# Kernel tuning notes

Hardware: AMD Instinct MI355X
Metric: run time of the kernel (lower is better)

Reference implementation:

```python
import math
import jax, jax.numpy as jnp
import numpy as np

NUM_EXPERTS = 8
TOP_K = 2
CAPACITY_FACTOR = 1.0
B, S, H, I = 4, 2048, 1024, 4096


def setup_inputs() -> dict:
    key = jax.random.key(0)
    k_x, k_rw, k_wi, k_wo = jax.random.split(key, 4)
    x = jax.random.normal(k_x, (B, S, H), dtype=jnp.float32)
    # router: nn.Linear(H, E), xavier_uniform weight, zero-ish bias
    lim = math.sqrt(6.0 / (H + NUM_EXPERTS))
    router_w = jax.random.uniform(k_rw, (NUM_EXPERTS, H), minval=-lim, maxval=lim, dtype=jnp.float32)
    router_b = jnp.zeros((NUM_EXPERTS,), dtype=jnp.float32)
    # expert weights (scaled randn for numerical sanity)
    experts_inter = jax.random.normal(k_wi, (NUM_EXPERTS - 1, H, I), dtype=jnp.float32) / math.sqrt(H)
    experts_out = jax.random.normal(k_wo, (NUM_EXPERTS - 1, I, H), dtype=jnp.float32) / math.sqrt(I)
    return {"x": x, "router_w": router_w, "router_b": router_b,
            "experts_inter": experts_inter, "experts_out": experts_out}


def reference(x, router_w, router_b, experts_inter, experts_out):
    batch, seq, hidden = x.shape
    n_exp = router_w.shape[0]
    n_tok = batch * seq
    cap = math.ceil(n_tok / n_exp * CAPACITY_FACTOR)  # expert capacity

    # router: linear + softmax
    logits = jnp.einsum('bsh,eh->bse', x, router_w) + router_b
    weights_flat = jax.nn.softmax(logits, axis=-1).reshape(n_tok, n_exp)
    x_flat = x.reshape(n_tok, hidden)

    # top-k gating; scatter topk values back into a dense [N, E] matrix
    topk_vals, topk_idx = jax.lax.top_k(weights_flat, TOP_K)
    rows = jnp.arange(n_tok)[:, None]
    topk_flat = jnp.zeros_like(weights_flat).at[rows, topk_idx].set(topk_vals)
    routing_mask = (topk_flat > 0).astype(jnp.int32)

    # no-op path = last expert column (identity * gate weight)
    noop_w = topk_flat[:, -1]
    noop_mask = routing_mask[:, -1].astype(x.dtype)

    # real experts: columns 0..E-2; capacity-limited dispatch via per-column sort
    expert_w = topk_flat[:, :-1]           # [N, E-1]
    expert_mask = routing_mask[:, :-1]     # [N, E-1]
    sorted_indices = jnp.argsort(-expert_mask, axis=0)[:cap]          # [cap, E-1]
    sorted_mask = jnp.take_along_axis(expert_mask, sorted_indices, axis=0)
    used_idx = (sorted_indices * sorted_mask).reshape(-1)             # masked -> index 0

    inputs = x_flat[used_idx] * sorted_mask.reshape(-1).astype(x.dtype)[:, None]
    inputs = inputs.reshape(cap, n_exp - 1, hidden)                   # [cap, E-1, H]
    in_w = jnp.take_along_axis(expert_w, sorted_indices, axis=0)      # [cap, E-1]

    # batched per-expert FFN
    h = jax.nn.relu(jnp.einsum('ceh,ehi->cei', inputs, experts_inter))
    out = jnp.einsum('cei,eih->ceh', h, experts_out) * in_w[..., None]

    # scatter-combine (masked slots write zeros into row 0, harmless)
    combined = jnp.zeros_like(x_flat).at[used_idx].add(out.reshape(-1, hidden))
    combined = combined + x_flat * (noop_w * noop_mask)[:, None]
    return combined.reshape(batch, seq, hidden)
```

## Files before the change

kernel.cpp:

```cpp
#include <hip/hip_runtime.h>
#include <hip/hip_bf16.h>
#include <stdint.h>
#include <stddef.h>


#define N_TOK   8192
#define HDIM    1024
#define IDIM    4096
#define NEXP    7
#define CAP     1024

typedef __bf16 bf16_t;
typedef bf16_t bf16x8 __attribute__((ext_vector_type(8)));
typedef float  f32x4  __attribute__((ext_vector_type(4)));

typedef __attribute__((address_space(3))) char lds_char_t;
typedef __attribute__((address_space(1))) const char glob_char_t;

__device__ __forceinline__ void load_lds16(const void* g, void* l) {
    __builtin_amdgcn_global_load_lds((glob_char_t*)(uintptr_t)g,
                                     (lds_char_t*)(uintptr_t)l, 16, 0, 0);
}

__device__ __forceinline__ bf16x8 pack8(const float* v) {
    bf16x8 r;
#pragma unroll
    for (int j = 0; j < 8; j++) r[j] = (bf16_t)v[j];
    return r;
}

__global__ __launch_bounds__(256) void router_kernel(
    const float* __restrict__ x, const float* __restrict__ rw,
    const float* __restrict__ rb, float* __restrict__ routew,
    float* __restrict__ out)
{
    const int wave = threadIdx.x >> 6, lane = threadIdx.x & 63;
    const int t = blockIdx.x * 4 + wave;
    const float4* xr = (const float4*)(x + (size_t)t * HDIM);
    float4 xv[4];
#pragma unroll
    for (int r = 0; r < 4; r++) xv[r] = xr[lane + r * 64];
    float p[8];
#pragma unroll
    for (int e = 0; e < 8; e++) {
        const float4* wr = (const float4*)(rw + (size_t)e * HDIM);
        float s = 0.f;
#pragma unroll
        for (int r = 0; r < 4; r++) {
            float4 wv = wr[lane + r * 64];
            s += xv[r].x * wv.x + xv[r].y * wv.y + xv[r].z * wv.z + xv[r].w * wv.w;
        }
#pragma unroll
        for (int o = 32; o; o >>= 1) s += __shfl_xor(s, o, 64);
        p[e] = s + rb[e];
    }
    float m = p[0];
#pragma unroll
    for (int e = 1; e < 8; e++) m = fmaxf(m, p[e]);
    float sum = 0.f;
#pragma unroll
    for (int e = 0; e < 8; e++) { p[e] = expf(p[e] - m); sum += p[e]; }
    float inv = 1.f / sum;
#pragma unroll
    for (int e = 0; e < 8; e++) p[e] *= inv;
    int i1 = 0;
#pragma unroll
    for (int e = 1; e < 8; e++) if (p[e] > p[i1]) i1 = e;
    int i2 = (i1 == 0) ? 1 : 0;
#pragma unroll
    for (int e = 0; e < 8; e++) if (e != i1 && p[e] > p[i2]) i2 = e;
    if (lane == 0) {
#pragma unroll
        for (int c = 0; c < 8; c++)
            routew[(size_t)t * 8 + c] = (c == i1) ? p[i1] : ((c == i2) ? p[i2] : 0.f);
    }
    const float c7 = (i1 == 7 || i2 == 7) ? p[7] : 0.f;
    float4* o = (float4*)(out + (size_t)t * HDIM);
#pragma unroll
    for (int r = 0; r < 4; r++) {
        float4 v = xv[r];
        v.x *= c7; v.y *= c7; v.z *= c7; v.w *= c7;
        o[lane + r * 64] = v;
    }
}

__global__ __launch_bounds__(1024) void compact_kernel(
    const float* __restrict__ routew, int* __restrict__ list,
    float* __restrict__ wsel)
{
    const int e = blockIdx.x;
    const int tid = threadIdx.x, wave = tid >> 6, lane = tid & 63;
    for (int i = tid; i < CAP; i += 1024) { list[e * CAP + i] = -1; wsel[e * CAP + i] = 0.f; }
    __shared__ int cnt[16];
    __syncthreads();
    int base = 0;
    const unsigned long long below = (lane == 63) ? ~0ull >> 1 : ((1ull << lane) - 1);
    for (int chunk = 0; chunk < N_TOK / 1024; chunk++) {
        const int t = chunk * 1024 + tid;
        const float w = routew[(size_t)t * 8 + e];
        const bool sel = (w > 0.f);
        const unsigned long long mask = __ballot(sel);
        const int rnk = __popcll(mask & below);
        if (lane == 0) cnt[wave] = __popcll(mask);
        __syncthreads();
        int pre = base;
        for (int w2 = 0; w2 < wave; w2++) pre += cnt[w2];
        const int rank = pre + rnk;
        if (sel && rank < CAP) { list[e * CAP + rank] = t; wsel[e * CAP + rank] = w; }
        int tot = 0;
        for (int w2 = 0; w2 < 16; w2++) tot += cnt[w2];
        base += tot;
        __syncthreads();
    }
}

__global__ __launch_bounds__(128) void gather_kernel(
    const float* __restrict__ x, const int* __restrict__ list,
    bf16_t* __restrict__ A)
{
    const int row = blockIdx.x;
    const int t = list[row];
    const int i = threadIdx.x;
    float4 v0 = {0.f, 0.f, 0.f, 0.f}, v1 = v0;
    if (t >= 0) {
        const float4* xs = (const float4*)(x + (size_t)t * HDIM);
        v0 = xs[i * 2];
        v1 = xs[i * 2 + 1];
    }
    bf16x8 o;
    o[0] = (bf16_t)v0.x; o[1] = (bf16_t)v0.y; o[2] = (bf16_t)v0.z; o[3] = (bf16_t)v0.w;
    o[4] = (bf16_t)v1.x; o[5] = (bf16_t)v1.y; o[6] = (bf16_t)v1.z; o[7] = (bf16_t)v1.w;
    ((bf16x8*)(A + (size_t)row * HDIM))[i] = o;
}

template<int K, int N>
__global__ __launch_bounds__(256) void transpose_cvt(
    const float* __restrict__ W, bf16_t* __restrict__ Wt)
{
    __shared__ float Ts[64][65];
    const int t = threadIdx.x;
    const int e = blockIdx.z;
    const int ktile = blockIdx.y * 64, ntile = blockIdx.x * 64;
    const float* We = W + (size_t)e * K * N;
    const int kr = t >> 4, nc = (t & 15) * 4;
#pragma unroll
    for (int j = 0; j < 4; j++) {
        const float4 v = *(const float4*)(We + (size_t)(ktile + kr + j * 16) * N + ntile + nc);
        Ts[nc + 0][kr + j * 16] = v.x;
        Ts[nc + 1][kr + j * 16] = v.y;
        Ts[nc + 2][kr + j * 16] = v.z;
        Ts[nc + 3][kr + j * 16] = v.w;
    }
    __syncthreads();
    const int n = t >> 2, kc = (t & 3) * 16;
    bf16_t* o = Wt + ((size_t)e * N + ntile + n) * K + ktile + kc;
    bf16x8 p0, p1;
#pragma unroll
    for (int i = 0; i < 8; i++) {
        p0[i] = (bf16_t)Ts[n][kc + i];
        p1[i] = (bf16_t)Ts[n][kc + 8 + i];
    }
    ((bf16x8*)o)[0] = p0;
    ((bf16x8*)o)[1] = p1;
}

template<int KDIM, int NDIM, int KSPLIT, bool IS_G1>
__global__ __launch_bounds__(256) void ffn_gemm_t(
    const bf16_t* __restrict__ Ab, const bf16_t* __restrict__ Bt,
    bf16_t* __restrict__ Hout, const int* __restrict__ list,
    const float* __restrict__ wsel, float* __restrict__ out)
{
    constexpr int BM = 128, BN = 128, BK = 32;
    constexpr int KLEN = KDIM / KSPLIT;
    constexpr int NT = KLEN / BK;
    constexpr int STG = 4096 + 4096;
    __shared__ __align__(16) bf16_t smem[3 * STG];
    const int tid = threadIdx.x, wave = tid >> 6, lane = tid & 63;

    const int gid = blockIdx.x;
    const int xcd = gid & 7, t5 = gid >> 3;
    int e, ks, mt, nt;
    if (IS_G1) {
        e  = t5 >> 5; ks = 0;
        mt = (t5 >> 2) & 7;
        nt = xcd * 4 + (t5 & 3);
    } else {
        const int ez = t5 >> 3, r5 = t5 & 7;
        e  = ez / KSPLIT; ks = ez % KSPLIT;
        nt = (xcd & 1) * 4 + (r5 & 3);
        mt = (xcd >> 1) * 2 + (r5 >> 2);
    }
    const int mblk = mt * BM, nblk = nt * BN;

    const bf16_t* Ae = Ab + ((size_t)e * CAP + mblk) * KDIM + (size_t)ks * KLEN;
    const bf16_t* Be = Bt + ((size_t)e * NDIM + nblk) * KDIM + (size_t)ks * KLEN;

    const int r = tid >> 2;
    const int cc = tid & 3;
    const int c = cc ^ ((r >> 1) & 3);
    const bf16_t* agA = Ae + (size_t)r * KDIM + c * 8;
    const bf16_t* agB = Be + (size_t)r * KDIM + c * 8;
    const int wbase = wave * 512;

    auto stage = [&](int koff, int s) {
        bf16_t* Ad = smem + s * STG + wbase;
        bf16_t* Bd = smem + s * STG + 4096 + wbase;
        load_lds16(agA + koff, Ad);
        load_lds16(agA + (size_t)64 * KDIM + koff, Ad + 2048);
        load_lds16(agB + koff, Bd);
        load_lds16(agB + (size_t)64 * KDIM + koff, Bd + 2048);
    };

    const int wm = (wave & 1) * 64, wn = (wave >> 1) * 64;
    const int lr = lane & 15, q = lane >> 4;
    const int sw = (q ^ ((lr >> 1) & 3)) * 8;

    f32x4 acc[4][4] = {};

    stage(0, 0);
    stage(BK, 1);

    int pb = 0;
    for (int kt = 0; kt < NT; kt++) {
        if (kt + 2 < NT) {
            int nb = pb + 2; if (nb >= 3) nb -= 3;
            stage((kt + 2) * BK, nb);
            asm volatile("s_waitcnt vmcnt(8)" ::: "memory");
        } else if (kt + 2 == NT) {
            asm volatile("s_waitcnt vmcnt(4)" ::: "memory");
        } else {
            asm volatile("s_waitcnt vmcnt(0)" ::: "memory");
        }
        asm volatile("s_barrier" ::: "memory");

        const bf16_t* Ap = smem + pb * STG;
        const bf16_t* Bp = smem + pb * STG + 4096;
        bf16x8 af[4], bfr[4];
#pragma unroll
        for (int i = 0; i < 4; i++)
            af[i] = *(const bf16x8*)(Ap + (wm + i * 16 + lr) * BK + sw);
#pragma unroll
        for (int j = 0; j < 4; j++)
            bfr[j] = *(const bf16x8*)(Bp + (wn + j * 16 + lr) * BK + sw);
#pragma unroll
        for (int i = 0; i < 4; i++)
#pragma unroll
            for (int j = 0; j < 4; j++)
                acc[i][j] = __builtin_amdgcn_mfma_f32_16x16x32_bf16(af[i], bfr[j], acc[i][j], 0, 0, 0);

        if (kt + 1 < NT) {
            asm volatile("s_waitcnt lgkmcnt(0)" ::: "memory");
            asm volatile("s_barrier" ::: "memory");
        }
        pb = (pb == 2) ? 0 : pb + 1;
    }

    if (IS_G1) {
        bf16_t* Ho = Hout + ((size_t)e * CAP + mblk) * NDIM + nblk;
#pragma unroll
        for (int i = 0; i < 4; i++) {
            const int r0 = wm + i * 16 + q * 4;
#pragma unroll
            for (int reg = 0; reg < 4; reg++) {
                bf16_t* row = Ho + (size_t)(r0 + reg) * NDIM;
#pragma unroll
                for (int j = 0; j < 4; j++)
                    row[wn + j * 16 + lr] = (bf16_t)fmaxf(acc[i][j][reg], 0.f);
            }
        }
    } else {
#pragma unroll
        for (int i = 0; i < 4; i++) {
            const int r0 = mblk + wm + i * 16 + q * 4;
#pragma unroll
            for (int reg = 0; reg < 4; reg++) {
                const int row = r0 + reg;
                const int tok = list[e * CAP + row];
                const float wgt = wsel[e * CAP + row];
                if (tok >= 0) {
                    float* orow = out + (size_t)tok * NDIM + nblk;
#pragma unroll
                    for (int j = 0; j < 4; j++)
                        atomicAdd(orow + wn + j * 16 + lr, acc[i][j][reg] * wgt);
                }
            }
        }
    }
}

template<int KDIM, int NDIM, bool IS_G1>
__global__ __launch_bounds__(256) void ffn_gemm_fused(
    const bf16_t* __restrict__ Ab, const float* __restrict__ Wb,
    bf16_t* __restrict__ Hout, const int* __restrict__ list,
    const float* __restrict__ wsel, float* __restrict__ out)
{
    constexpr int BM = 128, BN = 128, BK = 32;
    __shared__ __align__(16) bf16_t As[BM * BK];
    __shared__ __align__(16) bf16_t Bs[BN * BK];
    const int tid = threadIdx.x, wave = tid >> 6, lane = tid & 63;
    const int e = blockIdx.z, mblk = blockIdx.y * BM, nblk = blockIdx.x * BN;

    const bf16_t* Ae = Ab + ((size_t)e * CAP + mblk) * KDIM;
    const float*  We = Wb + (size_t)e * KDIM * NDIM + nblk;

    const int ar = tid >> 2, ac = (tid & 3) * 8;
    const bf16_t* ag0 = Ae + (size_t)ar * KDIM + ac;
    const bf16_t* ag1 = ag0 + (size_t)64 * KDIM;
    bf16_t* as0 = As + wave * 512;
    bf16_t* as1 = As + 2048 + wave * 512;

    const int bn = tid & 127, bc = (tid >> 7) * 2;
    const float* bg = We + bn;
    bf16_t* bsw0 = Bs + bn * BK + ((bc ^ (bn & 3)) * 8);
    bf16_t* bsw1 = Bs + bn * BK + (((bc + 1) ^ (bn & 3)) * 8);

    const int wm = (wave & 1) * 64, wn = (wave >> 1) * 64;
    const int lr = lane & 15, q = lane >> 4;
    const int swz = q ^ ((wn + lr) & 3);

    f32x4 acc[4][4] = {};

    for (int k0 = 0; k0 < KDIM; k0 += BK) {
        load_lds16(ag0 + k0, as0);
        load_lds16(ag1 + k0, as1);
        const float* bp = bg + (size_t)(k0 + bc * 8) * NDIM;
        float v[16];
#pragma unroll
        for (int j = 0; j < 16; j++) v[j] = bp[(size_t)j * NDIM];
        bf16x8 p0 = pack8(v), p1 = pack8(v + 8);
        *(bf16x8*)bsw0 = p0;
        *(bf16x8*)bsw1 = p1;
        __syncthreads();
        bf16x8 af[4], bfr[4];
#pragma unroll
        for (int i = 0; i < 4; i++)
            af[i] = *(const bf16x8*)(As + (wm + i * 16 + lr) * BK + q * 8);
#pragma unroll
        for (int j = 0; j < 4; j++)
            bfr[j] = *(const bf16x8*)(Bs + (wn + j * 16 + lr) * BK + swz * 8);
#pragma unroll
        for (int i = 0; i < 4; i++)
#pragma unroll
            for (int j = 0; j < 4; j++)
                acc[i][j] = __builtin_amdgcn_mfma_f32_16x16x32_bf16(af[i], bfr[j], acc[i][j], 0, 0, 0);
        __syncthreads();
    }

    if (IS_G1) {
        bf16_t* Ho = Hout + ((size_t)e * CAP + mblk) * NDIM + nblk;
#pragma unroll
        for (int i = 0; i < 4; i++) {
            const int r0 = wm + i * 16 + q * 4;
#pragma unroll
            for (int reg = 0; reg < 4; reg++) {
                bf16_t* row = Ho + (size_t)(r0 + reg) * NDIM;
#pragma unroll
                for (int j = 0; j < 4; j++)
                    row[wn + j * 16 + lr] = (bf16_t)fmaxf(acc[i][j][reg], 0.f);
            }
        }
    } else {
#pragma unroll
        for (int i = 0; i < 4; i++) {
            const int r0 = mblk + wm + i * 16 + q * 4;
#pragma unroll
            for (int reg = 0; reg < 4; reg++) {
                const int row = r0 + reg;
                const int tok = list[e * CAP + row];
                const float wgt = wsel[e * CAP + row];
                if (tok >= 0) {
                    float* orow = out + (size_t)tok * NDIM + nblk;
#pragma unroll
                    for (int j = 0; j < 4; j++)
                        atomicAdd(orow + wn + j * 16 + lr, acc[i][j][reg] * wgt);
                }
            }
        }
    }
}

extern "C" void kernel_launch(void* const* d_in, const int* in_sizes, int n_in,
                              void* d_out, int out_size, void* d_ws, size_t ws_size,
                              hipStream_t stream) {
    const float* x  = (const float*)d_in[0];
    const float* rw = (const float*)d_in[1];
    const float* rb = (const float*)d_in[2];
    const float* w1 = (const float*)d_in[3];
    const float* w2 = (const float*)d_in[4];
    float* out = (float*)d_out;

    char* ws = (char*)d_ws;
    float*  routew = (float*)(ws);
    int*    list   = (int*)(ws + 262144);
    float*  wsel   = (float*)(ws + 262144 + 28672);
    bf16_t* Abuf   = (bf16_t*)(ws + 319488);
    bf16_t* Hbuf   = (bf16_t*)(ws + 14999552);
    bf16_t* Wt     = (bf16_t*)(ws + 73719808);

    const size_t NEED = 73719808ull + 58720256ull;

    router_kernel<<<N_TOK / 4, 256, 0, stream>>>(x, rw, rb, routew, out);
    compact_kernel<<<NEXP, 1024, 0, stream>>>(routew, list, wsel);
    gather_kernel<<<NEXP * CAP, 128, 0, stream>>>(x, list, Abuf);

    if (ws_size >= NEED) {
        transpose_cvt<HDIM, IDIM><<<dim3(IDIM / 64, HDIM / 64, NEXP), 256, 0, stream>>>(w1, Wt);
        ffn_gemm_t<HDIM, IDIM, 1, true><<<1792, 256, 0, stream>>>(
            Abuf, Wt, Hbuf, nullptr, nullptr, nullptr);
        transpose_cvt<IDIM, HDIM><<<dim3(HDIM / 64, IDIM / 64, NEXP), 256, 0, stream>>>(w2, Wt);
        ffn_gemm_t<IDIM, HDIM, 2, false><<<896, 256, 0, stream>>>(
            Hbuf, Wt, nullptr, list, wsel, out);
    } else {
        ffn_gemm_fused<HDIM, IDIM, true><<<dim3(IDIM / 128, CAP / 128, NEXP), 256, 0, stream>>>(
            Abuf, w1, Hbuf, nullptr, nullptr, nullptr);
        ffn_gemm_fused<IDIM, HDIM, false><<<dim3(HDIM / 128, CAP / 128, NEXP), 256, 0, stream>>>(
            Hbuf, w2, nullptr, list, wsel, out);
    }
}
```

Baseline: 494.2 us.

## Enlarge GEMM tile to 256x128 with 8 waves, double buffering, split-K 4

The expert FFN GEMM kernel now uses 512-thread blocks with a 256x128 output tile, so each B tile is reused across twice as many rows. The LDS pipeline drops from three stages to two to fit the larger tile. The block-to-tile mapping is rewritten, and the second GEMM's split-K goes from 2 to 4 to keep 896 blocks in flight. The aim is less global/LDS traffic per FLOP, at the cost of a shallower prefetch pipeline and more atomic partial-sum traffic in the second GEMM.

```diff
diff --git a/kernel.cpp b/kernel.cpp
--- a/kernel.cpp
+++ b/kernel.cpp
@@ -165,76 +165,69 @@
 }
 
 template<int KDIM, int NDIM, int KSPLIT, bool IS_G1>
-__global__ __launch_bounds__(256) void ffn_gemm_t(
+__global__ __launch_bounds__(512, 4) void ffn_gemm_t(
     const bf16_t* __restrict__ Ab, const bf16_t* __restrict__ Bt,
     bf16_t* __restrict__ Hout, const int* __restrict__ list,
     const float* __restrict__ wsel, float* __restrict__ out)
 {
-    constexpr int BM = 128, BN = 128, BK = 32;
+    constexpr int BM = 256, BN = 128, BK = 32;
     constexpr int KLEN = KDIM / KSPLIT;
     constexpr int NT = KLEN / BK;
-    constexpr int STG = 4096 + 4096;
-    __shared__ __align__(16) bf16_t smem[3 * STG];
+    constexpr int SA = BM * BK;
+    constexpr int STG = SA + BN * BK;
+    __shared__ __align__(16) bf16_t smem[2 * STG];
     const int tid = threadIdx.x, wave = tid >> 6, lane = tid & 63;
 
-    const int gid = blockIdx.x;
-    const int xcd = gid & 7, t5 = gid >> 3;
-    int e, ks, mt, nt;
+    const int gid = blockIdx.x, xcd = gid & 7, t5 = gid >> 3;
+    int e, ks, mblk, nblk;
     if (IS_G1) {
-        e  = t5 >> 5; ks = 0;
-        mt = (t5 >> 2) & 7;
-        nt = xcd * 4 + (t5 & 3);
+        e = t5 >> 4; const int rem = t5 & 15;
+        ks = 0;
+        mblk = (rem >> 2) * BM;
+        nblk = (xcd * 4 + (rem & 3)) * BN;
     } else {
-        const int ez = t5 >> 3, r5 = t5 & 7;
-        e  = ez / KSPLIT; ks = ez % KSPLIT;
-        nt = (xcd & 1) * 4 + (r5 & 3);
-        mt = (xcd >> 1) * 2 + (r5 >> 2);
-    }
-    const int mblk = mt * BM, nblk = nt * BN;
+        e = t5 >> 4; const int rem = t5 & 15;
+        ks = rem >> 2;
+        mblk = (rem & 3) * BM;
+        nblk = xcd * BN;
+    }
 
     const bf16_t* Ae = Ab + ((size_t)e * CAP + mblk) * KDIM + (size_t)ks * KLEN;
     const bf16_t* Be = Bt + ((size_t)e * NDIM + nblk) * KDIM + (size_t)ks * KLEN;
 
-    const int r = tid >> 2;
-    const int cc = tid & 3;
-    const int c = cc ^ ((r >> 1) & 3);
-    const bf16_t* agA = Ae + (size_t)r * KDIM + c * 8;
-    const bf16_t* agB = Be + (size_t)r * KDIM + c * 8;
-    const int wbase = wave * 512;
+    const int ar = lane >> 2;
+    const int ac8 = ((lane & 3) ^ ((lane >> 3) & 3)) * 8;
+    const bf16_t* agA0 = Ae + (size_t)(32 * wave + ar) * KDIM + ac8;
+    const bf16_t* agA1 = agA0 + (size_t)16 * KDIM;
+    const bf16_t* agB  = Be + (size_t)(16 * wave + ar) * KDIM + ac8;
 
     auto stage = [&](int koff, int s) {
-        bf16_t* Ad = smem + s * STG + wbase;
-        bf16_t* Bd = smem + s * STG + 4096 + wbase;
-        load_lds16(agA + koff, Ad);
-        load_lds16(agA + (size_t)64 * KDIM + koff, Ad + 2048);
-        load_lds16(agB + koff, Bd);
-        load_lds16(agB + (size_t)64 * KDIM + koff, Bd + 2048);
+        bf16_t* base = smem + s * STG;
+        load_lds16(agA0 + koff, base + wave * 1024);
+        load_lds16(agA1 + koff, base + wave * 1024 + 512);
+        load_lds16(agB + koff, base + SA + wave * 512);
     };
 
-    const int wm = (wave & 1) * 64, wn = (wave >> 1) * 64;
+    const int wm = (wave & 3) * 64, wn = (wave >> 2) * 64;
     const int lr = lane & 15, q = lane >> 4;
     const int sw = (q ^ ((lr >> 1) & 3)) * 8;
 
     f32x4 acc[4][4] = {};
 
     stage(0, 0);
-    stage(BK, 1);
-
-    int pb = 0;
-    for (int kt = 0; kt < NT; kt++) {
-        if (kt + 2 < NT) {
-            int nb = pb + 2; if (nb >= 3) nb -= 3;
-            stage((kt + 2) * BK, nb);
-            asm volatile("s_waitcnt vmcnt(8)" ::: "memory");
-        } else if (kt + 2 == NT) {
-            asm volatile("s_waitcnt vmcnt(4)" ::: "memory");
+
+    int p = 0;
+    for (int kt = 0; kt < NT; kt++, p ^= 1) {
+        if (kt + 1 < NT) {
+            stage((kt + 1) * BK, p ^ 1);
+            asm volatile("s_waitcnt vmcnt(3)" ::: "memory");
         } else {
             asm volatile("s_waitcnt vmcnt(0)" ::: "memory");
         }
         asm volatile("s_barrier" ::: "memory");
 
-        const bf16_t* Ap = smem + pb * STG;
-        const bf16_t* Bp = smem + pb * STG + 4096;
+        const bf16_t* Ap = smem + p * STG;
+        const bf16_t* Bp = smem + p * STG + SA;
         bf16x8 af[4], bfr[4];
 #pragma unroll
         for (int i = 0; i < 4; i++)
@@ -252,7 +245,6 @@
             asm volatile("s_waitcnt lgkmcnt(0)" ::: "memory");
             asm volatile("s_barrier" ::: "memory");
         }
-        pb = (pb == 2) ? 0 : pb + 1;
     }
 
     if (IS_G1) {
@@ -405,10 +397,10 @@
 
     if (ws_size >= NEED) {
         transpose_cvt<HDIM, IDIM><<<dim3(IDIM / 64, HDIM / 64, NEXP), 256, 0, stream>>>(w1, Wt);
-        ffn_gemm_t<HDIM, IDIM, 1, true><<<1792, 256, 0, stream>>>(
+        ffn_gemm_t<HDIM, IDIM, 1, true><<<896, 512, 0, stream>>>(
             Abuf, Wt, Hbuf, nullptr, nullptr, nullptr);
         transpose_cvt<IDIM, HDIM><<<dim3(HDIM / 64, IDIM / 64, NEXP), 256, 0, stream>>>(w2, Wt);
-        ffn_gemm_t<IDIM, HDIM, 2, false><<<896, 256, 0, stream>>>(
+        ffn_gemm_t<IDIM, HDIM, 4, false><<<896, 512, 0, stream>>>(
             Hbuf, Wt, nullptr, list, wsel, out);
     } else {
         ffn_gemm_fused<HDIM, IDIM, true><<<dim3(IDIM / 128, CAP / 128, NEXP), 256, 0, stream>>>(
```

Result: slower. 525.9 us (+6.4%).
